# Kernel optimization log

Measured on AMD Instinct MI355X. Metric: run time of the kernel, lower is better.

Reference implementation:

```python
import jax, jax.numpy as jnp
import numpy as np

WIN = 5                # win_size
DT = (WIN - 1) // 2    # delta_t
OUT_DIM = 64


def setup_inputs() -> dict:
    key = jax.random.key(0)
    k1, k2, k3 = jax.random.split(key, 3)
    N, C, J, T = 64, 16, 25, 120
    c = C + 1                      # + time channel (signatory.Augment include_time=True)
    sig_ch = c + c * c             # signature_channels(c, depth=2)
    x = jax.random.normal(k1, (N, C, J, T), jnp.float32)
    W = jax.random.normal(k2, (sig_ch, OUT_DIM), jnp.float32) * 0.05
    b = jax.random.normal(k3, (OUT_DIM,), jnp.float32) * 0.05
    return {"x": x, "W": W, "b": b}


def _window_increments(x):
    # Boundary windows are shorter (clip); we emulate them by clipping indices so
    # out-of-range slots duplicate the endpoint -> zero increments -> identity in
    # the tensor algebra, leaving the signature unchanged (faithful to the ragged loop).
    N, C, J, T = x.shape
    t = jnp.arange(T)
    pos = t[:, None] + (jnp.arange(WIN) - DT)[None, :]
    start = jnp.maximum(t - DT, 0)
    end = jnp.minimum(t + DT + 1, T)
    L = (end - start).astype(jnp.float32)                     # window length, >= DT+1
    pc = jnp.clip(pos, 0, T - 1)
    xp = jnp.transpose(x, (0, 2, 3, 1))                       # [N,J,T,C]
    pts = xp[:, :, pc, :]
    # signatory time channel = linspace(0,1,L) over the valid window;
    # duplicated boundary slots share the endpoint's time (zero increment)
    time = (pc - start[:, None]).astype(jnp.float32) / (L[:, None] - 1.0)
    time_b = jnp.broadcast_to(time[None, None, :, :, None], (N, J, T, WIN, 1))
    path = jnp.concatenate([pts, time_b], axis=-1)
    path = jnp.concatenate([jnp.zeros_like(path[..., :1, :]), path], axis=-2)  # basepoint=True
    return jnp.diff(path, axis=-2)


def _signature_depth2(inc):
    c = inc.shape[-1]
    lead = inc.shape[:-2]
    S1 = jnp.zeros(lead + (c,), inc.dtype)
    S2 = jnp.zeros(lead + (c, c), inc.dtype)

    def step(carry, v):
        S1, S2 = carry
        S2 = S2 + S1[..., :, None] * v[..., None, :] + 0.5 * (v[..., :, None] * v[..., None, :])
        S1 = S1 + v
        return (S1, S2), None

    (S1, S2), _ = jax.lax.scan(step, (S1, S2), jnp.moveaxis(inc, -2, 0))
    return S1, S2


def reference(x, W, b):
    inc = _window_increments(x)
    S1, S2 = _signature_depth2(inc)                           # [N,J,T,c], [N,J,T,c,c]
    y = jnp.concatenate([S1, S2.reshape(S2.shape[:-2] + (-1,))], axis=-1)  # [N,J,T,306]
    z = jnp.einsum('njts,so->njto', y, W) + b                 # Linear
    return jnp.transpose(z, (0, 3, 1, 2))                     # [N,out_dim,J,T]
```

## Files before the change

### kernel.cpp

```cpp
#include <hip/hip_runtime.h>
#include <hip/hip_fp16.h>

#define J_DIM 25
#define T_DIM 120
#define O_DIM 64
#define KPAD  328
#define TB    64
#define XPADH 24

typedef _Float16 f16x8 __attribute__((ext_vector_type(8)));
typedef __attribute__((ext_vector_type(4))) float f32x4;

__device__ __forceinline__ unsigned h2bits(__half2 h) {
    unsigned u; __builtin_memcpy(&u, &h, 4); return u;
}
__device__ __forceinline__ __half2 bits2h(unsigned u) {
    __half2 h; __builtin_memcpy(&h, &u, 4); return h;
}
__device__ __forceinline__ __half2 sel4h(int q, __half2 a, __half2 b, __half2 c, __half2 d) {
    unsigned s01 = (q & 1) ? h2bits(b) : h2bits(a);
    unsigned s23 = (q & 1) ? h2bits(d) : h2bits(c);
    return bits2h((q & 2) ? s23 : s01);
}

__global__ void wprep(const float* __restrict__ W, __half* __restrict__ Wf) {
    int i = blockIdx.x * 256 + threadIdx.x;
    if (i >= O_DIM * KPAD) return;
    int o = i / KPAD, k = i % KPAD;
    int a = k / 18, b = k % 18;
    float v = 0.0f;
    if (k < 306) v = (b == 17) ? W[a * O_DIM + o] : 0.5f * W[(17 + 17 * a + b) * O_DIM + o];
    Wf[o * KPAD + k] = __float2half(v);
}

__global__ __launch_bounds__(256, 2) void sig_mfma(
    const float* __restrict__ x, const __half* __restrict__ Wf,
    const float* __restrict__ bias, float* __restrict__ out)
{
    __shared__ __half xs[4][20][XPADH];
    __shared__ __half ys[TB * KPAD];

    const int tid = threadIdx.x;
    const int bid = blockIdx.x;
    const int half_ = bid & 1;
    const int j = (bid >> 1) % J_DIM;
    const int n = bid / (2 * J_DIM);
    const int t0 = half_ * 56;
    const int wave = tid >> 6, lane = tid & 63;
    const int l15 = lane & 15, l4 = lane >> 4;
    const int t0w = t0 + wave * 16;

    const float* xbase = x + ((size_t)(n * 16) * J_DIM + j) * T_DIM;
    #pragma unroll
    for (int k = 0; k < 5; ++k) {
        int idx = lane + k * 64;
        int c = idx / 20, i = idx % 20;
        int st = min(max(t0w - 2 + i, 0), T_DIM - 1);
        xs[wave][i][c] = __float2half(xbase[(size_t)c * J_DIM * T_DIM + st]);
    }
    if (lane < 48) {
        int r = lane / 3, p = lane % 3;
        *(uint4*)((char*)ys + (wave * 16 + r) * 656 + 608 + p * 16) = uint4{0, 0, 0, 0};
    }
    __builtin_amdgcn_wave_barrier();

    {
        const int row = tid >> 2, qg = tid & 3;
        const int rloc = lane >> 2;
        const int t = t0 + row;
        const int start = max(t - 2, 0), end = min(t + 3, T_DIM);
        const float inv = 1.0f / (float)(end - start - 1);
        float ptvf[5];
        #pragma unroll
        for (int w = 0; w < 5; ++w) {
            int pcw = min(max(t - 2 + w, 0), T_DIM - 1);
            ptvf[w] = (float)(pcw - start) * inv;
        }
        __half2 ptvb[5];
        #pragma unroll
        for (int w = 0; w < 5; ++w) ptvb[w] = __float2half2_rn(ptvf[w]);

        __half2 xw[5][8];
        #pragma unroll
        for (int w = 0; w < 5; ++w) {
            uint4 lo = *(const uint4*)&xs[wave][rloc + w][0];
            uint4 hi = *(const uint4*)&xs[wave][rloc + w][8];
            xw[w][0] = bits2h(lo.x); xw[w][1] = bits2h(lo.y);
            xw[w][2] = bits2h(lo.z); xw[w][3] = bits2h(lo.w);
            xw[w][4] = bits2h(hi.x); xw[w][5] = bits2h(hi.y);
            xw[w][6] = bits2h(hi.z); xw[w][7] = bits2h(hi.w);
        }

        {
            __half2 pr[5];
            #pragma unroll
            for (int w = 0; w < 5; ++w)
                pr[w] = sel4h(qg, xw[w][0], xw[w][1], xw[w][2], xw[w][3]);
            __half2 hp[5];
            hp[0] = __hneg2(pr[1]);
            hp[1] = __hsub2(pr[0], pr[2]);
            hp[2] = __hsub2(pr[1], pr[3]);
            hp[3] = __hsub2(pr[2], pr[4]);
            hp[4] = __hadd2(pr[3], pr[4]);
            __half2 h0b[5], h1b[5];
            #pragma unroll
            for (int w = 0; w < 5; ++w) {
                h0b[w] = __low2half2(hp[w]);
                h1b[w] = __high2half2(hp[w]);
            }
            unsigned u0[9], u1[9];
            #pragma unroll
            for (int b2 = 0; b2 < 8; ++b2) {
                __half2 a0 = __hmul2(h0b[0], xw[0][b2]);
                __half2 a1 = __hmul2(h1b[0], xw[0][b2]);
                #pragma unroll
                for (int w = 1; w < 5; ++w) {
                    a0 = __hfma2(h0b[w], xw[w][b2], a0);
                    a1 = __hfma2(h1b[w], xw[w][b2], a1);
                }
                u0[b2] = h2bits(a0);
                u1[b2] = h2bits(a1);
            }
            {
                __half2 a16 = __hmul2(hp[0], ptvb[0]);
                #pragma unroll
                for (int w = 1; w < 5; ++w) a16 = __hfma2(hp[w], ptvb[w], a16);
                u0[8] = h2bits(__halves2half2(__low2half(a16),  __low2half(pr[4])));
                u1[8] = h2bits(__halves2half2(__high2half(a16), __high2half(pr[4])));
            }
            char* yr = (char*)ys + row * 656 + 72 * qg;
            *(uint2*)(yr +  0) = uint2{u0[0], u0[1]};
            *(uint2*)(yr +  8) = uint2{u0[2], u0[3]};
            *(uint2*)(yr + 16) = uint2{u0[4], u0[5]};
            *(uint2*)(yr + 24) = uint2{u0[6], u0[7]};
            *(uint2*)(yr + 32) = uint2{u0[8], u1[0]};
            *(uint2*)(yr + 40) = uint2{u1[1], u1[2]};
            *(uint2*)(yr + 48) = uint2{u1[3], u1[4]};
            *(uint2*)(yr + 56) = uint2{u1[5], u1[6]};
            *(uint2*)(yr + 64) = uint2{u1[7], u1[8]};
        }

        {
            __half2 pr[5];
            #pragma unroll
            for (int w = 0; w < 5; ++w)
                pr[w] = sel4h(qg, xw[w][4], xw[w][5], xw[w][6], xw[w][7]);
            __half2 hp[5];
            hp[0] = __hneg2(pr[1]);
            hp[1] = __hsub2(pr[0], pr[2]);
            hp[2] = __hsub2(pr[1], pr[3]);
            hp[3] = __hsub2(pr[2], pr[4]);
            hp[4] = __hadd2(pr[3], pr[4]);
            __half2 h0b[5], h1b[5];
            #pragma unroll
            for (int w = 0; w < 5; ++w) {
                h0b[w] = __low2half2(hp[w]);
                h1b[w] = __high2half2(hp[w]);
            }
            unsigned u0[9], u1[9];
            #pragma unroll
            for (int b2 = 0; b2 < 8; ++b2) {
                __half2 a0 = __hmul2(h0b[0], xw[0][b2]);
                __half2 a1 = __hmul2(h1b[0], xw[0][b2]);
                #pragma unroll
                for (int w = 1; w < 5; ++w) {
                    a0 = __hfma2(h0b[w], xw[w][b2], a0);
                    a1 = __hfma2(h1b[w], xw[w][b2], a1);
                }
                u0[b2] = h2bits(a0);
                u1[b2] = h2bits(a1);
            }
            {
                __half2 a16 = __hmul2(hp[0], ptvb[0]);
                #pragma unroll
                for (int w = 1; w < 5; ++w) a16 = __hfma2(hp[w], ptvb[w], a16);
                u0[8] = h2bits(__halves2half2(__low2half(a16),  __low2half(pr[4])));
                u1[8] = h2bits(__halves2half2(__high2half(a16), __high2half(pr[4])));
            }
            char* yr = (char*)ys + row * 656 + 72 * qg + 288;
            *(uint2*)(yr +  0) = uint2{u0[0], u0[1]};
            *(uint2*)(yr +  8) = uint2{u0[2], u0[3]};
            *(uint2*)(yr + 16) = uint2{u0[4], u0[5]};
            *(uint2*)(yr + 24) = uint2{u0[6], u0[7]};
            *(uint2*)(yr + 32) = uint2{u0[8], u1[0]};
            *(uint2*)(yr + 40) = uint2{u1[1], u1[2]};
            *(uint2*)(yr + 48) = uint2{u1[3], u1[4]};
            *(uint2*)(yr + 56) = uint2{u1[5], u1[6]};
            *(uint2*)(yr + 64) = uint2{u1[7], u1[8]};
        }

        if (qg == 0) {
            __half2 htb[5];
            htb[0] = __float2half2_rn(-ptvf[1]);
            htb[1] = __float2half2_rn(ptvf[0] - ptvf[2]);
            htb[2] = __float2half2_rn(ptvf[1] - ptvf[3]);
            htb[3] = __float2half2_rn(ptvf[2] - ptvf[4]);
            htb[4] = __float2half2_rn(ptvf[3] + ptvf[4]);
            unsigned ut[9];
            #pragma unroll
            for (int b2 = 0; b2 < 8; ++b2) {
                __half2 a = __hmul2(htb[0], xw[0][b2]);
                #pragma unroll
                for (int w = 1; w < 5; ++w) a = __hfma2(htb[w], xw[w][b2], a);
                ut[b2] = h2bits(a);
            }
            {
                __half2 a = __hmul2(htb[0], ptvb[0]);
                #pragma unroll
                for (int w = 1; w < 5; ++w) a = __hfma2(htb[w], ptvb[w], a);
                ut[8] = h2bits(__halves2half2(__low2half(a), __float2half(ptvf[4])));
            }
            char* yt = (char*)ys + row * 656 + 576;
            *(uint2*)(yt +  0) = uint2{ut[0], ut[1]};
            *(uint2*)(yt +  8) = uint2{ut[2], ut[3]};
            *(uint2*)(yt + 16) = uint2{ut[4], ut[5]};
            *(uint2*)(yt + 24) = uint2{ut[6], ut[7]};
            *(unsigned*)(yt + 32) = ut[8];
        }
    }
    __syncthreads();

    {
        const float bv = bias[wave * 16 + l15];
        const __half* Bb = Wf + (size_t)(wave * 16 + l15) * KPAD + l4 * 8;
        f16x8 bfrag[10];
        #pragma unroll
        for (int kk = 0; kk < 10; ++kk)
            bfrag[kk] = *(const f16x8*)(Bb + kk * 32);
        #pragma unroll
        for (int mi = 0; mi < 4; ++mi) {
            const char* Ab = (const char*)ys + (mi * 16 + l15) * 656 + l4 * 16;
            f32x4 acc = f32x4{bv, bv, bv, bv};
            #pragma unroll
            for (int kk = 0; kk < 10; ++kk) {
                f16x8 af = *(const f16x8*)(Ab + kk * 64);
                acc = __builtin_amdgcn_mfma_f32_16x16x32_f16(af, bfrag[kk], acc, 0, 0, 0);
            }
            const int tg = t0 + mi * 16 + l4 * 4;
            float* op = out + ((size_t)(n * O_DIM + wave * 16 + l15) * J_DIM + j) * T_DIM + tg;
            *(f32x4*)op = acc;
        }
    }
}

extern "C" void kernel_launch(void* const* d_in, const int* in_sizes, int n_in,
                              void* d_out, int out_size, void* d_ws, size_t ws_size,
                              hipStream_t stream) {
    const float* x = (const float*)d_in[0];
    const float* W = (const float*)d_in[1];
    const float* b = (const float*)d_in[2];
    float* out = (float*)d_out;
    __half* Wf = (__half*)d_ws;

    wprep<<<(O_DIM * KPAD + 255) / 256, 256, 0, stream>>>(W, Wf);
    sig_mfma<<<64 * J_DIM * 2, 256, 0, stream>>>(x, Wf, b, out);
}
```

Before: 33.14 us.

## Split time-channel build across lane groups and start MFMA on own rows before barrier

The time-channel row block, previously built only by lane group 0, is now spread across all four lane groups, each writing one 8-byte chunk. Each wave then issues the MFMA tile for the rows it built itself, after only a wave-level barrier, before the block-wide __syncthreads, so part of the matmul overlaps other waves' signature work. The remaining three row tiles are processed after the barrier in a rotated order. This relies on each wave writing exactly the 16 LDS rows it then reads; if that mapping does not hold, results are wrong.

Result: no change. 33.67 us (+1.6%).

```diff
diff --git a/kernel.cpp b/kernel.cpp
--- a/kernel.cpp
+++ b/kernel.cpp
@@ -189,57 +189,71 @@
             *(uint2*)(yr + 64) = uint2{u1[7], u1[8]};
         }
 
-        if (qg == 0) {
+        {
             __half2 htb[5];
             htb[0] = __float2half2_rn(-ptvf[1]);
             htb[1] = __float2half2_rn(ptvf[0] - ptvf[2]);
             htb[2] = __float2half2_rn(ptvf[1] - ptvf[3]);
             htb[3] = __float2half2_rn(ptvf[2] - ptvf[4]);
             htb[4] = __float2half2_rn(ptvf[3] + ptvf[4]);
-            unsigned ut[9];
-            #pragma unroll
-            for (int b2 = 0; b2 < 8; ++b2) {
-                __half2 a = __hmul2(htb[0], xw[0][b2]);
-                #pragma unroll
-                for (int w = 1; w < 5; ++w) a = __hfma2(htb[w], xw[w][b2], a);
-                ut[b2] = h2bits(a);
-            }
-            {
+            __half2 pba = sel4h(qg, xw[0][0], xw[0][2], xw[0][4], xw[0][6]);
+            __half2 pbb = sel4h(qg, xw[0][1], xw[0][3], xw[0][5], xw[0][7]);
+            __half2 aa = __hmul2(htb[0], pba);
+            __half2 ab = __hmul2(htb[0], pbb);
+            #pragma unroll
+            for (int w = 1; w < 5; ++w) {
+                __half2 qa = sel4h(qg, xw[w][0], xw[w][2], xw[w][4], xw[w][6]);
+                __half2 qb = sel4h(qg, xw[w][1], xw[w][3], xw[w][5], xw[w][7]);
+                aa = __hfma2(htb[w], qa, aa);
+                ab = __hfma2(htb[w], qb, ab);
+            }
+            char* yt = (char*)ys + row * 656 + 576;
+            *(uint2*)(yt + 8 * qg) = uint2{h2bits(aa), h2bits(ab)};
+            if (qg == 0) {
                 __half2 a = __hmul2(htb[0], ptvb[0]);
                 #pragma unroll
                 for (int w = 1; w < 5; ++w) a = __hfma2(htb[w], ptvb[w], a);
-                ut[8] = h2bits(__halves2half2(__low2half(a), __float2half(ptvf[4])));
-            }
-            char* yt = (char*)ys + row * 656 + 576;
-            *(uint2*)(yt +  0) = uint2{ut[0], ut[1]};
-            *(uint2*)(yt +  8) = uint2{ut[2], ut[3]};
-            *(uint2*)(yt + 16) = uint2{ut[4], ut[5]};
-            *(uint2*)(yt + 24) = uint2{ut[6], ut[7]};
-            *(unsigned*)(yt + 32) = ut[8];
-        }
+                *(unsigned*)(yt + 32) =
+                    h2bits(__halves2half2(__low2half(a), __float2half(ptvf[4])));
+            }
+        }
+    }
+    __builtin_amdgcn_wave_barrier();
+
+    const float bv = bias[wave * 16 + l15];
+    const __half* Bb = Wf + (size_t)(wave * 16 + l15) * KPAD + l4 * 8;
+    f16x8 bfrag[10];
+    #pragma unroll
+    for (int kk = 0; kk < 10; ++kk)
+        bfrag[kk] = *(const f16x8*)(Bb + kk * 32);
+    {
+        const int mi = wave;
+        const char* Ab = (const char*)ys + (mi * 16 + l15) * 656 + l4 * 16;
+        f32x4 acc = f32x4{bv, bv, bv, bv};
+        #pragma unroll
+        for (int kk = 0; kk < 10; ++kk) {
+            f16x8 af = *(const f16x8*)(Ab + kk * 64);
+            acc = __builtin_amdgcn_mfma_f32_16x16x32_f16(af, bfrag[kk], acc, 0, 0, 0);
+        }
+        const int tg = t0 + mi * 16 + l4 * 4;
+        float* op = out + ((size_t)(n * O_DIM + wave * 16 + l15) * J_DIM + j) * T_DIM + tg;
+        *(f32x4*)op = acc;
     }
     __syncthreads();
 
-    {
-        const float bv = bias[wave * 16 + l15];
-        const __half* Bb = Wf + (size_t)(wave * 16 + l15) * KPAD + l4 * 8;
-        f16x8 bfrag[10];
-        #pragma unroll
-        for (int kk = 0; kk < 10; ++kk)
-            bfrag[kk] = *(const f16x8*)(Bb + kk * 32);
-        #pragma unroll
-        for (int mi = 0; mi < 4; ++mi) {
-            const char* Ab = (const char*)ys + (mi * 16 + l15) * 656 + l4 * 16;
-            f32x4 acc = f32x4{bv, bv, bv, bv};
-            #pragma unroll
-            for (int kk = 0; kk < 10; ++kk) {
-                f16x8 af = *(const f16x8*)(Ab + kk * 64);
-                acc = __builtin_amdgcn_mfma_f32_16x16x32_f16(af, bfrag[kk], acc, 0, 0, 0);
-            }
-            const int tg = t0 + mi * 16 + l4 * 4;
-            float* op = out + ((size_t)(n * O_DIM + wave * 16 + l15) * J_DIM + j) * T_DIM + tg;
-            *(f32x4*)op = acc;
-        }
+    #pragma unroll
+    for (int d = 1; d < 4; ++d) {
+        const int mi = (wave + d) & 3;
+        const char* Ab = (const char*)ys + (mi * 16 + l15) * 656 + l4 * 16;
+        f32x4 acc = f32x4{bv, bv, bv, bv};
+        #pragma unroll
+        for (int kk = 0; kk < 10; ++kk) {
+            f16x8 af = *(const f16x8*)(Ab + kk * 64);
+            acc = __builtin_amdgcn_mfma_f32_16x16x32_f16(af, bfrag[kk], acc, 0, 0, 0);
+        }
+        const int tg = t0 + mi * 16 + l4 * 4;
+        float* op = out + ((size_t)(n * O_DIM + wave * 16 + l15) * J_DIM + j) * T_DIM + tg;
+        *(f32x4*)op = acc;
     }
 }
 
```
